# Performance work log

Hardware: AMD Instinct MI355X
Metric: run time of the kernel (lower is better)

Reference implementation:

```python
import jax, jax.numpy as jnp
import numpy as np

B, S, D, H = 2, 2048, 1024, 16
HD = D // H
LN_EPS = 1e-5


def setup_inputs() -> dict:
    key = jax.random.key(0)
    ks = jax.random.split(key, 8)
    inv = 1.0 / np.sqrt(D)
    return {
        "embedded": jax.random.normal(ks[0], (B, S, D), dtype=jnp.float32),
        "Wq": jax.random.normal(ks[1], (D, D), dtype=jnp.float32) * inv,
        "bq": jax.random.normal(ks[2], (D,), dtype=jnp.float32) * 0.01,
        "Wk": jax.random.normal(ks[3], (D, D), dtype=jnp.float32) * inv,
        "bk": jax.random.normal(ks[4], (D,), dtype=jnp.float32) * 0.01,
        "Wv": jax.random.normal(ks[5], (D, D), dtype=jnp.float32) * inv,
        "bv": jax.random.normal(ks[6], (D,), dtype=jnp.float32) * 0.01,
        "gamma": jnp.ones((D,), dtype=jnp.float32),
        "beta": jnp.zeros((D,), dtype=jnp.float32),
    }


def reference(embedded, Wq, bq, Wk, bk, Wv, bv, gamma, beta):
    b, s, d = embedded.shape
    # QKV projections (torch Linear: x @ W^T + b)
    q = embedded @ Wq.T + bq
    k = embedded @ Wk.T + bk
    v = embedded @ Wv.T + bv
    # [b, s, H, hd] -> [b, H, s, hd]
    q = q.reshape(b, s, H, HD).transpose(0, 2, 1, 3)
    k = k.reshape(b, s, H, HD).transpose(0, 2, 1, 3)
    v = v.reshape(b, s, H, HD).transpose(0, 2, 1, 3)
    # scores [b, H, s, s]
    qk = jnp.einsum("bhqd,bhkd->bhqk", q, k)
    # NaN scrub -> -inf (original: qk[qk != qk] = -inf)
    qk = jnp.where(jnp.isnan(qk), -jnp.inf, qk)
    # NOTE: original scales by sqrt(shape[-1]) == sqrt(seq_len), not head_dim
    qk = qk / jnp.float32(np.sqrt(s))
    p = jax.nn.softmax(qk, axis=-1)
    p = jnp.where(jnp.isnan(p), 0.0, p)
    v = jnp.where(jnp.isnan(v), 0.0, v)
    # post-softmax upper-triangular (incl. diagonal) mask, no renormalization
    mask = jnp.triu(jnp.ones((s, s), dtype=p.dtype), k=0)
    p = p * mask
    z = jnp.einsum("bhqk,bhkd->bhqd", p, v)  # [b, H, s, hd]
    # original does a raw .view(b, s, -1) on contiguous [b,h,s,hd] (no transpose)
    z = z.reshape(b, s, d)
    # residual + LayerNorm
    x = embedded + z
    mu = jnp.mean(x, axis=-1, keepdims=True)
    var = jnp.mean(jnp.square(x - mu), axis=-1, keepdims=True)
    out = (x - mu) * jax.lax.rsqrt(var + LN_EPS) * gamma + beta
    return out
```

## Files before the change

kernel.cpp:

```cpp
#include <hip/hip_runtime.h>
#include <hip/hip_bf16.h>
#include <math.h>

typedef unsigned short ushort_t;
typedef unsigned char uchar_t;
typedef __attribute__((ext_vector_type(8))) short short8;
typedef __attribute__((ext_vector_type(4))) float f32x4;

struct __align__(8) us4 { ushort_t u[4]; };

__device__ __forceinline__ ushort_t f2bf(float x) {
  union { float f; unsigned u; } c; c.f = x;
  unsigned r = c.u + 0x7FFFu + ((c.u >> 16) & 1u);
  return (ushort_t)(r >> 16);
}
__device__ __forceinline__ float bf2f(ushort_t b) {
  union { unsigned u; float f; } c; c.u = ((unsigned)b) << 16;
  return c.f;
}

__global__ __launch_bounds__(256) void cvt_kernel(const float* __restrict__ src,
                                                  ushort_t* __restrict__ dst, int n) {
  int i = (blockIdx.x * 256 + threadIdx.x) * 4;
  if (i < n) {
    f32x4 v = *(const f32x4*)(src + i);
    us4 o;
    o.u[0] = f2bf(v[0]); o.u[1] = f2bf(v[1]); o.u[2] = f2bf(v[2]); o.u[3] = f2bf(v[3]);
    *(us4*)(dst + i) = o;
  }
}

struct QkvArgs {
  const ushort_t* X;
  const ushort_t* W0; const ushort_t* W1; const ushort_t* W2;
  const float* b0; const float* b1; const float* b2;
  ushort_t* o0; ushort_t* o1; ushort_t* o2;
};

__global__ __launch_bounds__(256) void qkv_gemm(QkvArgs a) {
  __shared__ __align__(16) ushort_t As[128 * 32];
  __shared__ __align__(16) ushort_t Bs[128 * 32];
  const int z = blockIdx.z;
  const ushort_t* W  = (z == 0) ? a.W0 : ((z == 1) ? a.W1 : a.W2);
  const float* bias  = (z == 0) ? a.b0 : ((z == 1) ? a.b1 : a.b2);
  ushort_t* out      = (z == 0) ? a.o0 : ((z == 1) ? a.o1 : a.o2);
  const int swz = (z == 1) ? 7 : 0;
  const int mBase = blockIdx.x * 128;
  const int nBase = blockIdx.y * 128;
  const int tid  = threadIdx.x;
  const int lane = tid & 63;
  const int w    = tid >> 6;
  const int wm   = w >> 1, wn = w & 1;
  const int quad = lane >> 4;
  const int l15  = lane & 15;

  f32x4 acc[4][4] = {};

  const int srow = lane >> 2;
  const int scol = (lane & 3) * 8;
  const ushort_t* gA0 = a.X + (mBase + srow) * 1024 + scol;
  const ushort_t* gB0 = W   + (nBase + srow) * 1024 + scol;

  for (int k0 = 0; k0 < 1024; k0 += 32) {
#pragma unroll
    for (int p = 0; p < 2; ++p) {
      int rr = (w * 2 + p) * 16;
      __builtin_amdgcn_global_load_lds(
          (const __attribute__((address_space(1))) void*)(gA0 + rr * 1024 + k0),
          (__attribute__((address_space(3))) void*)(As + (w * 2 + p) * 512), 16, 0, 0);
      __builtin_amdgcn_global_load_lds(
          (const __attribute__((address_space(1))) void*)(gB0 + rr * 1024 + k0),
          (__attribute__((address_space(3))) void*)(Bs + (w * 2 + p) * 512), 16, 0, 0);
    }
    __syncthreads();
    short8 af[4], bfr[4];
#pragma unroll
    for (int mi = 0; mi < 4; ++mi)
      af[mi] = *(const short8*)(As + (wm * 64 + mi * 16 + l15) * 32 + quad * 8);
#pragma unroll
    for (int ni = 0; ni < 4; ++ni)
      bfr[ni] = *(const short8*)(Bs + (wn * 64 + ni * 16 + l15) * 32 + quad * 8);
#pragma unroll
    for (int mi = 0; mi < 4; ++mi)
#pragma unroll
      for (int ni = 0; ni < 4; ++ni)
        acc[mi][ni] = __builtin_amdgcn_mfma_f32_16x16x32_bf16(af[mi], bfr[ni], acc[mi][ni], 0, 0, 0);
    __syncthreads();
  }

#pragma unroll
  for (int ni = 0; ni < 4; ++ni) {
    int n = nBase + wn * 64 + ni * 16 + l15;
    float bv = bias[n];
    int h = n >> 6, hd = n & 63;
    int hdHi = hd >> 3, hdLo = hd & 7;
#pragma unroll
    for (int mi = 0; mi < 4; ++mi) {
      int m0 = mBase + wm * 64 + mi * 16 + quad * 4;
#pragma unroll
      for (int r = 0; r < 4; ++r) {
        int m = m0 + r;
        int bb = m >> 11, s = m & 2047;
        int hdw = (((hdHi ^ (s & swz)) << 3) | hdLo);
        out[((bb * 16 + h) * 2048 + s) * 64 + hdw] = f2bf(acc[mi][ni][r] + bv);
      }
    }
  }
}

__global__ __launch_bounds__(256) void tr_kernel(const ushort_t* __restrict__ vb,
                                                 uchar_t* __restrict__ vT) {
  __shared__ uchar_t Ls[64 * 68];
  int bh = blockIdx.y;
  int s0 = blockIdx.x * 64;
  int tid = threadIdx.x;
  const ushort_t* vp = vb + (size_t)bh * 131072;
  uchar_t* op = vT + (size_t)bh * 131072;
#pragma unroll
  for (int p = 0; p < 2; ++p) {
    int c = p * 256 + tid;
    int row = c >> 3, u = c & 7;
    short8 x = *(const short8*)(vp + (size_t)(s0 + row) * 64 + u * 8);
    float f0 = bf2f((ushort_t)x[0]), f1 = bf2f((ushort_t)x[1]);
    float f2 = bf2f((ushort_t)x[2]), f3 = bf2f((ushort_t)x[3]);
    float f4 = bf2f((ushort_t)x[4]), f5 = bf2f((ushort_t)x[5]);
    float f6 = bf2f((ushort_t)x[6]), f7 = bf2f((ushort_t)x[7]);
    unsigned int lo = __builtin_amdgcn_cvt_pk_fp8_f32(f0, f1, 0, false);
    lo = __builtin_amdgcn_cvt_pk_fp8_f32(f2, f3, lo, true);
    unsigned int hi = __builtin_amdgcn_cvt_pk_fp8_f32(f4, f5, 0, false);
    hi = __builtin_amdgcn_cvt_pk_fp8_f32(f6, f7, hi, true);
    *(unsigned int*)(Ls + row * 68 + u * 8)     = lo;
    *(unsigned int*)(Ls + row * 68 + u * 8 + 4) = hi;
  }
  __syncthreads();
#pragma unroll
  for (int p = 0; p < 4; ++p) {
    int oc = p * 256 + tid;
    int hd = oc >> 4, sc = oc & 15;
    unsigned int v = 0;
#pragma unroll
    for (int i = 0; i < 4; ++i)
      v |= ((unsigned int)Ls[(sc * 4 + i) * 68 + hd]) << (8 * i);
    int u = ((s0 & 64) >> 4) + (sc >> 2);
    int dest = (s0 & ~127) + ((u ^ (hd & 7)) * 16) + (sc & 3) * 4;
    *(unsigned int*)(op + (size_t)hd * 2048 + dest) = v;
  }
}

__global__ __launch_bounds__(256) void attn_kernel(const ushort_t* __restrict__ qb,
                                                   const ushort_t* __restrict__ kb,
                                                   const uchar_t* __restrict__ vT,
                                                   ushort_t* __restrict__ zb) {
  __shared__ __align__(16) ushort_t Ks[128 * 64];
  __shared__ __align__(16) uchar_t  Vt[64 * 128];
  __shared__ __align__(16) uchar_t  Ps[128 * 128];
  const int bh   = blockIdx.y;
  const int qblk = blockIdx.x * 128;
  const int tid  = threadIdx.x;
  const int lane = tid & 63;
  const int w    = tid >> 6;
  const int quad = lane >> 4;
  const int l15  = lane & 15;
  const int l7   = l15 & 7;
  const float cexp = 0.02209708691f * 1.44269504089f;

  const ushort_t* qpage = qb + (size_t)bh * (2048 * 64);
  const ushort_t* kpage = kb + (size_t)bh * (2048 * 64);
  const uchar_t*  vpage = vT + (size_t)bh * (64 * 2048);

  short8 qf[2][2];
#pragma unroll
  for (int nb = 0; nb < 2; ++nb) {
    int qg = qblk + w * 32 + nb * 16 + l15;
#pragma unroll
    for (int kd = 0; kd < 2; ++kd)
      qf[nb][kd] = *(const short8*)(qpage + (size_t)qg * 64 + kd * 32 + quad * 8);
  }

  float psum[2] = {0.f, 0.f};
  f32x4 o[4][2] = {};

  for (int kt = 0; kt < 2048; kt += 128) {
    const bool needV = (kt + 127 >= qblk);
    const bool needP = (kt + 127 >= qblk + w * 32);
    __syncthreads();

#pragma unroll
    for (int p = 0; p < 4; ++p) {
      int j = w * 4 + p;
      __builtin_amdgcn_global_load_lds(
          (const __attribute__((address_space(1))) void*)(kpage + (size_t)kt * 64 + j * 512 + lane * 8),
          (__attribute__((address_space(3))) void*)(Ks + j * 512), 16, 0, 0);
    }
    if (needV) {
#pragma unroll
      for (int p = 0; p < 2; ++p) {
        int j = w * 2 + p;
        __builtin_amdgcn_global_load_lds(
            (const __attribute__((address_space(1))) void*)(vpage + (size_t)(j * 8 + (lane >> 3)) * 2048 + kt + (lane & 7) * 16),
            (__attribute__((address_space(3))) void*)(Vt + j * 1024), 16, 0, 0);
      }
    }
    __syncthreads();

#pragma unroll
    for (int mb = 0; mb < 8; ++mb) {
      const ushort_t* krow = Ks + (mb * 16 + l15) * 64;
      short8 kf0 = *(const short8*)(krow + ((0 + quad) ^ l7) * 8);
      short8 kf1 = *(const short8*)(krow + ((4 + quad) ^ l7) * 8);
      f32x4 s0 = {}, s1 = {};
      s0 = __builtin_amdgcn_mfma_f32_16x16x32_bf16(kf0, qf[0][0], s0, 0, 0, 0);
      s0 = __builtin_amdgcn_mfma_f32_16x16x32_bf16(kf1, qf[0][1], s0, 0, 0, 0);
      s1 = __builtin_amdgcn_mfma_f32_16x16x32_bf16(kf0, qf[1][0], s1, 0, 0, 0);
      s1 = __builtin_amdgcn_mfma_f32_16x16x32_bf16(kf1, qf[1][1], s1, 0, 0, 0);
      const int keyb = kt + mb * 16 + quad * 4;
#pragma unroll
      for (int nb = 0; nb < 2; ++nb) {
        f32x4 s = nb ? s1 : s0;
        float p0 = __builtin_amdgcn_exp2f(s[0] * cexp);
        float p1 = __builtin_amdgcn_exp2f(s[1] * cexp);
        float p2 = __builtin_amdgcn_exp2f(s[2] * cexp);
        float p3 = __builtin_amdgcn_exp2f(s[3] * cexp);
        psum[nb] += (p0 + p1) + (p2 + p3);
        if (needP) {
          int qg = qblk + w * 32 + nb * 16 + l15;
          float m0 = (keyb + 0 >= qg) ? p0 : 0.f;
          float m1 = (keyb + 1 >= qg) ? p1 : 0.f;
          float m2 = (keyb + 2 >= qg) ? p2 : 0.f;
          float m3 = (keyb + 3 >= qg) ? p3 : 0.f;
          unsigned int pk = __builtin_amdgcn_cvt_pk_fp8_f32(m0, m1, 0, false);
          pk = __builtin_amdgcn_cvt_pk_fp8_f32(m2, m3, pk, true);
          *(unsigned int*)(Ps + (w * 32 + nb * 16 + l15) * 128 + ((mb ^ l7) * 16) + quad * 4) = pk;
        }
      }
    }

    if (needP) {
#pragma unroll
      for (int kd = 0; kd < 4; ++kd) {
        const int un = ((kd * 2 + (quad >> 1)) ^ l7) * 16 + (quad & 1) * 8;
        long long pf0 = *(const long long*)(Ps + (w * 32 + l15) * 128 + un);
        long long pf1 = *(const long long*)(Ps + (w * 32 + 16 + l15) * 128 + un);
#pragma unroll
        for (int mb = 0; mb < 4; ++mb) {
          long long vf = *(const long long*)(Vt + (mb * 16 + l15) * 128 + un);
          o[mb][0] = __builtin_amdgcn_mfma_f32_16x16x32_fp8_fp8(vf, pf0, o[mb][0], 0, 0, 0);
          o[mb][1] = __builtin_amdgcn_mfma_f32_16x16x32_fp8_fp8(vf, pf1, o[mb][1], 0, 0, 0);
        }
      }
    }
  }

#pragma unroll
  for (int nb = 0; nb < 2; ++nb) {
    psum[nb] += __shfl_xor(psum[nb], 16, 64);
    psum[nb] += __shfl_xor(psum[nb], 32, 64);
    float rl = 1.0f / psum[nb];
    int qg = qblk + w * 32 + nb * 16 + l15;
#pragma unroll
    for (int mb = 0; mb < 4; ++mb)
#pragma unroll
      for (int r = 0; r < 4; ++r) {
        int hd = mb * 16 + quad * 4 + r;
        zb[((size_t)bh * 2048 + qg) * 64 + hd] = f2bf(o[mb][nb][r] * rl);
      }
  }
}

__global__ __launch_bounds__(256) void ln_kernel(const float* __restrict__ emb,
                                                 const ushort_t* __restrict__ zb,
                                                 const float* __restrict__ gamma,
                                                 const float* __restrict__ beta,
                                                 float* __restrict__ out) {
  __shared__ float red[2][4];
  int row = blockIdx.x;
  int b = row >> 11, s = row & 2047;
  int h = s >> 7;
  int siHi = (s & 127) << 4;
  int tid = threadIdx.x;
  int dcol = tid * 4;
  int si = siHi | (dcol >> 6);
  int j = dcol & 63;

  f32x4 e4 = *(const f32x4*)(emb + (size_t)row * 1024 + dcol);
  us4 z4 = *(const us4*)(zb + (((size_t)(b * 16 + h) * 2048 + si) * 64 + j));
  float x0 = e4[0] + bf2f(z4.u[0]);
  float x1 = e4[1] + bf2f(z4.u[1]);
  float x2 = e4[2] + bf2f(z4.u[2]);
  float x3 = e4[3] + bf2f(z4.u[3]);

  float sum = x0 + x1 + x2 + x3;
  float sq  = x0 * x0 + x1 * x1 + x2 * x2 + x3 * x3;
#pragma unroll
  for (int off = 1; off <= 32; off <<= 1) {
    sum += __shfl_xor(sum, off, 64);
    sq  += __shfl_xor(sq,  off, 64);
  }
  int wv = tid >> 6;
  if ((tid & 63) == 0) { red[0][wv] = sum; red[1][wv] = sq; }
  __syncthreads();
  float ts = red[0][0] + red[0][1] + red[0][2] + red[0][3];
  float tq = red[1][0] + red[1][1] + red[1][2] + red[1][3];
  float mu = ts * (1.0f / 1024.0f);
  float var = tq * (1.0f / 1024.0f) - mu * mu;
  float rsig = rsqrtf(var + 1e-5f);

  f32x4 g4 = *(const f32x4*)(gamma + dcol);
  f32x4 b4 = *(const f32x4*)(beta + dcol);
  f32x4 o4;
  o4[0] = (x0 - mu) * rsig * g4[0] + b4[0];
  o4[1] = (x1 - mu) * rsig * g4[1] + b4[1];
  o4[2] = (x2 - mu) * rsig * g4[2] + b4[2];
  o4[3] = (x3 - mu) * rsig * g4[3] + b4[3];
  *(f32x4*)(out + (size_t)row * 1024 + dcol) = o4;
}

extern "C" void kernel_launch(void* const* d_in, const int* in_sizes, int n_in,
                              void* d_out, int out_size, void* d_ws, size_t ws_size,
                              hipStream_t stream) {
  (void)in_sizes; (void)n_in; (void)out_size; (void)ws_size;
  const float* emb   = (const float*)d_in[0];
  const float* Wq    = (const float*)d_in[1];
  const float* bq    = (const float*)d_in[2];
  const float* Wk    = (const float*)d_in[3];
  const float* bk    = (const float*)d_in[4];
  const float* Wv    = (const float*)d_in[5];
  const float* bv    = (const float*)d_in[6];
  const float* gamma = (const float*)d_in[7];
  const float* beta  = (const float*)d_in[8];
  float* out = (float*)d_out;

  char* ws = (char*)d_ws;
  ushort_t* Xbf  = (ushort_t*)(ws);
  ushort_t* Wqb  = (ushort_t*)(ws + 8388608);
  ushort_t* Wkb  = (ushort_t*)(ws + 10485760);
  ushort_t* Wvb  = (ushort_t*)(ws + 12582912);
  ushort_t* qbuf = (ushort_t*)(ws + 14680064);
  ushort_t* kbuf = (ushort_t*)(ws + 23068672);
  ushort_t* vbuf = (ushort_t*)(ws + 31457280);
  ushort_t* zbuf = (ushort_t*)(ws + 31457280);
  uchar_t*  vTb  = (uchar_t*)(ws + 39845888);

  cvt_kernel<<<4096, 256, 0, stream>>>(emb, Xbf, 4194304);
  cvt_kernel<<<1024, 256, 0, stream>>>(Wq, Wqb, 1048576);
  cvt_kernel<<<1024, 256, 0, stream>>>(Wk, Wkb, 1048576);
  cvt_kernel<<<1024, 256, 0, stream>>>(Wv, Wvb, 1048576);

  QkvArgs a;
  a.X = Xbf;
  a.W0 = Wqb; a.W1 = Wkb; a.W2 = Wvb;
  a.b0 = bq;  a.b1 = bk;  a.b2 = bv;
  a.o0 = qbuf; a.o1 = kbuf; a.o2 = vbuf;
  qkv_gemm<<<dim3(32, 8, 3), 256, 0, stream>>>(a);

  tr_kernel<<<dim3(32, 32), 256, 0, stream>>>(vbuf, vTb);

  attn_kernel<<<dim3(16, 32), 256, 0, stream>>>(qbuf, kbuf, vTb, zbuf);

  ln_kernel<<<4096, 256, 0, stream>>>(emb, zbuf, gamma, beta, out);
}
```

Measured before the change: 197.8 us.

## Split attention key range across two blocks and combine partial outputs

Attention is split along the key dimension into two halves via a third grid dimension, each writing a normalized bf16 partial output and its row sum. A new combine kernel merges the halves weighted by their sums. This doubles the number of attention blocks to improve GPU occupancy and load balance. The cost is an extra launch, extra partial-output memory traffic, and an extra bf16 rounding. It is only enabled when the workspace is large enough.

```diff
diff --git a/kernel.cpp b/kernel.cpp
--- a/kernel.cpp
+++ b/kernel.cpp
@@ -150,11 +150,16 @@
 __global__ __launch_bounds__(256) void attn_kernel(const ushort_t* __restrict__ qb,
                                                    const ushort_t* __restrict__ kb,
                                                    const uchar_t* __restrict__ vT,
-                                                   ushort_t* __restrict__ zb) {
+                                                   ushort_t* __restrict__ outO,
+                                                   float* __restrict__ outPs,
+                                                   int split) {
   __shared__ __align__(16) ushort_t Ks[128 * 64];
   __shared__ __align__(16) uchar_t  Vt[64 * 128];
   __shared__ __align__(16) uchar_t  Ps[128 * 128];
   const int bh   = blockIdx.y;
+  const int half = blockIdx.z;
+  const int kz   = half * 1024;
+  const int kend = split ? (kz + 1024) : 2048;
   const int qblk = blockIdx.x * 128;
   const int tid  = threadIdx.x;
   const int lane = tid & 63;
@@ -180,7 +185,7 @@
   float psum[2] = {0.f, 0.f};
   f32x4 o[4][2] = {};
 
-  for (int kt = 0; kt < 2048; kt += 128) {
+  for (int kt = kz; kt < kend; kt += 128) {
     const bool needV = (kt + 127 >= qblk);
     const bool needP = (kt + 127 >= qblk + w * 32);
     __syncthreads();
@@ -257,14 +262,38 @@
     psum[nb] += __shfl_xor(psum[nb], 32, 64);
     float rl = 1.0f / psum[nb];
     int qg = qblk + w * 32 + nb * 16 + l15;
+    size_t base = (((size_t)(half * 32 + bh) * 2048) + qg) * 64;
 #pragma unroll
     for (int mb = 0; mb < 4; ++mb)
 #pragma unroll
       for (int r = 0; r < 4; ++r) {
         int hd = mb * 16 + quad * 4 + r;
-        zb[((size_t)bh * 2048 + qg) * 64 + hd] = f2bf(o[mb][nb][r] * rl);
-      }
-  }
+        outO[base + hd] = f2bf(o[mb][nb][r] * rl);
+      }
+    if (split && quad == 0)
+      outPs[(half * 32 + bh) * 2048 + qg] = psum[nb];
+  }
+}
+
+__global__ __launch_bounds__(256) void comb_kernel(const ushort_t* __restrict__ Op,
+                                                   const float* __restrict__ Psm,
+                                                   ushort_t* __restrict__ zb) {
+  int t = blockIdx.x * 256 + threadIdx.x;
+  int chunk = t & 15;
+  int q  = (t >> 4) & 2047;
+  int bh = t >> 15;
+  float ps0 = Psm[bh * 2048 + q];
+  float ps1 = Psm[(32 + bh) * 2048 + q];
+  float rt = 1.0f / (ps0 + ps1);
+  size_t i0 = (((size_t)bh * 2048) + q) * 64 + chunk * 4;
+  size_t i1 = (((size_t)(32 + bh) * 2048) + q) * 64 + chunk * 4;
+  us4 a = *(const us4*)(Op + i0);
+  us4 b = *(const us4*)(Op + i1);
+  us4 r;
+#pragma unroll
+  for (int j = 0; j < 4; ++j)
+    r.u[j] = f2bf((ps0 * bf2f(a.u[j]) + ps1 * bf2f(b.u[j])) * rt);
+  *(us4*)(zb + i0) = r;
 }
 
 __global__ __launch_bounds__(256) void ln_kernel(const float* __restrict__ emb,
@@ -318,7 +347,7 @@
 extern "C" void kernel_launch(void* const* d_in, const int* in_sizes, int n_in,
                               void* d_out, int out_size, void* d_ws, size_t ws_size,
                               hipStream_t stream) {
-  (void)in_sizes; (void)n_in; (void)out_size; (void)ws_size;
+  (void)in_sizes; (void)n_in; (void)out_size;
   const float* emb   = (const float*)d_in[0];
   const float* Wq    = (const float*)d_in[1];
   const float* bq    = (const float*)d_in[2];
@@ -340,6 +369,9 @@
   ushort_t* vbuf = (ushort_t*)(ws + 31457280);
   ushort_t* zbuf = (ushort_t*)(ws + 31457280);
   uchar_t*  vTb  = (uchar_t*)(ws + 39845888);
+  ushort_t* Opart = (ushort_t*)(ws + 44040192);
+  float*    Psum  = (float*)(ws + 77594624);
+  const bool split = ws_size >= 78118912u;
 
   cvt_kernel<<<4096, 256, 0, stream>>>(emb, Xbf, 4194304);
   cvt_kernel<<<1024, 256, 0, stream>>>(Wq, Wqb, 1048576);
@@ -355,7 +387,12 @@
 
   tr_kernel<<<dim3(32, 32), 256, 0, stream>>>(vbuf, vTb);
 
-  attn_kernel<<<dim3(16, 32), 256, 0, stream>>>(qbuf, kbuf, vTb, zbuf);
+  if (split) {
+    attn_kernel<<<dim3(16, 32, 2), 256, 0, stream>>>(qbuf, kbuf, vTb, Opart, Psum, 1);
+    comb_kernel<<<4096, 256, 0, stream>>>(Opart, Psum, zbuf);
+  } else {
+    attn_kernel<<<dim3(16, 32, 1), 256, 0, stream>>>(qbuf, kbuf, vTb, zbuf, (float*)ws, 0);
+  }
 
   ln_kernel<<<4096, 256, 0, stream>>>(emb, zbuf, gamma, beta, out);
 }
```

After: 202.5 us. 1.02x slower.

## Double-buffer K and V tiles in LDS to prefetch the next key block

Applied to the files above, without the earlier changes.

The attention kernel now keeps two LDS buffers each for the K and V tiles. It issues the async global-to-LDS loads for the next 128-key block right after the barrier, then computes on the current block. This is meant to hide global load latency behind the QK^T, softmax and PV MFMA work, and it drops one barrier per iteration. In exchange LDS use per block rises from about 40KB to 64KB, which could limit occupancy, and the compiler may insert conservative vmcnt waits before LDS reads that cancel the overlap.

```diff
diff --git a/kernel.cpp b/kernel.cpp
--- a/kernel.cpp
+++ b/kernel.cpp
@@ -151,8 +151,8 @@
                                                    const ushort_t* __restrict__ kb,
                                                    const uchar_t* __restrict__ vT,
                                                    ushort_t* __restrict__ zb) {
-  __shared__ __align__(16) ushort_t Ks[128 * 64];
-  __shared__ __align__(16) uchar_t  Vt[64 * 128];
+  __shared__ __align__(16) ushort_t Ks[2][128 * 64];
+  __shared__ __align__(16) uchar_t  Vt[2][64 * 128];
   __shared__ __align__(16) uchar_t  Ps[128 * 128];
   const int bh   = blockIdx.y;
   const int qblk = blockIdx.x * 128;
@@ -180,72 +180,97 @@
   float psum[2] = {0.f, 0.f};
   f32x4 o[4][2] = {};
 
-  for (int kt = 0; kt < 2048; kt += 128) {
-    const bool needV = (kt + 127 >= qblk);
-    const bool needP = (kt + 127 >= qblk + w * 32);
-    __syncthreads();
-
-#pragma unroll
-    for (int p = 0; p < 4; ++p) {
-      int j = w * 4 + p;
+#pragma unroll
+  for (int p = 0; p < 4; ++p) {
+    int j = w * 4 + p;
+    __builtin_amdgcn_global_load_lds(
+        (const __attribute__((address_space(1))) void*)(kpage + (size_t)j * 512 + lane * 8),
+        (__attribute__((address_space(3))) void*)(Ks[0] + j * 512), 16, 0, 0);
+  }
+  if (127 >= qblk) {
+#pragma unroll
+    for (int p = 0; p < 2; ++p) {
+      int j = w * 2 + p;
       __builtin_amdgcn_global_load_lds(
-          (const __attribute__((address_space(1))) void*)(kpage + (size_t)kt * 64 + j * 512 + lane * 8),
-          (__attribute__((address_space(3))) void*)(Ks + j * 512), 16, 0, 0);
+          (const __attribute__((address_space(1))) void*)(vpage + (size_t)(j * 8 + (lane >> 3)) * 2048 + (lane & 7) * 16),
+          (__attribute__((address_space(3))) void*)(Vt[0] + j * 1024), 16, 0, 0);
     }
-    if (needV) {
-#pragma unroll
-      for (int p = 0; p < 2; ++p) {
-        int j = w * 2 + p;
-        __builtin_amdgcn_global_load_lds(
-            (const __attribute__((address_space(1))) void*)(vpage + (size_t)(j * 8 + (lane >> 3)) * 2048 + kt + (lane & 7) * 16),
-            (__attribute__((address_space(3))) void*)(Vt + j * 1024), 16, 0, 0);
-      }
-    }
-    __syncthreads();
-
-#pragma unroll
-    for (int mb = 0; mb < 8; ++mb) {
-      const ushort_t* krow = Ks + (mb * 16 + l15) * 64;
-      short8 kf0 = *(const short8*)(krow + ((0 + quad) ^ l7) * 8);
-      short8 kf1 = *(const short8*)(krow + ((4 + quad) ^ l7) * 8);
-      f32x4 s0 = {}, s1 = {};
-      s0 = __builtin_amdgcn_mfma_f32_16x16x32_bf16(kf0, qf[0][0], s0, 0, 0, 0);
-      s0 = __builtin_amdgcn_mfma_f32_16x16x32_bf16(kf1, qf[0][1], s0, 0, 0, 0);
-      s1 = __builtin_amdgcn_mfma_f32_16x16x32_bf16(kf0, qf[1][0], s1, 0, 0, 0);
-      s1 = __builtin_amdgcn_mfma_f32_16x16x32_bf16(kf1, qf[1][1], s1, 0, 0, 0);
-      const int keyb = kt + mb * 16 + quad * 4;
-#pragma unroll
-      for (int nb = 0; nb < 2; ++nb) {
-        f32x4 s = nb ? s1 : s0;
-        float p0 = __builtin_amdgcn_exp2f(s[0] * cexp);
-        float p1 = __builtin_amdgcn_exp2f(s[1] * cexp);
-        float p2 = __builtin_amdgcn_exp2f(s[2] * cexp);
-        float p3 = __builtin_amdgcn_exp2f(s[3] * cexp);
-        psum[nb] += (p0 + p1) + (p2 + p3);
-        if (needP) {
-          int qg = qblk + w * 32 + nb * 16 + l15;
-          float m0 = (keyb + 0 >= qg) ? p0 : 0.f;
-          float m1 = (keyb + 1 >= qg) ? p1 : 0.f;
-          float m2 = (keyb + 2 >= qg) ? p2 : 0.f;
-          float m3 = (keyb + 3 >= qg) ? p3 : 0.f;
-          unsigned int pk = __builtin_amdgcn_cvt_pk_fp8_f32(m0, m1, 0, false);
-          pk = __builtin_amdgcn_cvt_pk_fp8_f32(m2, m3, pk, true);
-          *(unsigned int*)(Ps + (w * 32 + nb * 16 + l15) * 128 + ((mb ^ l7) * 16) + quad * 4) = pk;
+  }
+
+  for (int kt2 = 0; kt2 < 2048; kt2 += 256) {
+#pragma unroll
+    for (int ph = 0; ph < 2; ++ph) {
+      const int kt = kt2 + ph * 128;
+      const ushort_t* KsB = Ks[ph];
+      const uchar_t*  VtB = Vt[ph];
+      const bool needP = (kt + 127 >= qblk + w * 32);
+
+      __syncthreads();
+
+      const int ktn = kt + 128;
+      if (ktn < 2048) {
+#pragma unroll
+        for (int p = 0; p < 4; ++p) {
+          int j = w * 4 + p;
+          __builtin_amdgcn_global_load_lds(
+              (const __attribute__((address_space(1))) void*)(kpage + (size_t)ktn * 64 + j * 512 + lane * 8),
+              (__attribute__((address_space(3))) void*)(Ks[ph ^ 1] + j * 512), 16, 0, 0);
         }
-      }
-    }
-
-    if (needP) {
-#pragma unroll
-      for (int kd = 0; kd < 4; ++kd) {
-        const int un = ((kd * 2 + (quad >> 1)) ^ l7) * 16 + (quad & 1) * 8;
-        long long pf0 = *(const long long*)(Ps + (w * 32 + l15) * 128 + un);
-        long long pf1 = *(const long long*)(Ps + (w * 32 + 16 + l15) * 128 + un);
-#pragma unroll
-        for (int mb = 0; mb < 4; ++mb) {
-          long long vf = *(const long long*)(Vt + (mb * 16 + l15) * 128 + un);
-          o[mb][0] = __builtin_amdgcn_mfma_f32_16x16x32_fp8_fp8(vf, pf0, o[mb][0], 0, 0, 0);
-          o[mb][1] = __builtin_amdgcn_mfma_f32_16x16x32_fp8_fp8(vf, pf1, o[mb][1], 0, 0, 0);
+        if (ktn + 127 >= qblk) {
+#pragma unroll
+          for (int p = 0; p < 2; ++p) {
+            int j = w * 2 + p;
+            __builtin_amdgcn_global_load_lds(
+                (const __attribute__((address_space(1))) void*)(vpage + (size_t)(j * 8 + (lane >> 3)) * 2048 + ktn + (lane & 7) * 16),
+                (__attribute__((address_space(3))) void*)(Vt[ph ^ 1] + j * 1024), 16, 0, 0);
+          }
+        }
+      }
+
+#pragma unroll
+      for (int mb = 0; mb < 8; ++mb) {
+        const ushort_t* krow = KsB + (mb * 16 + l15) * 64;
+        short8 kf0 = *(const short8*)(krow + ((0 + quad) ^ l7) * 8);
+        short8 kf1 = *(const short8*)(krow + ((4 + quad) ^ l7) * 8);
+        f32x4 s0 = {}, s1 = {};
+        s0 = __builtin_amdgcn_mfma_f32_16x16x32_bf16(kf0, qf[0][0], s0, 0, 0, 0);
+        s0 = __builtin_amdgcn_mfma_f32_16x16x32_bf16(kf1, qf[0][1], s0, 0, 0, 0);
+        s1 = __builtin_amdgcn_mfma_f32_16x16x32_bf16(kf0, qf[1][0], s1, 0, 0, 0);
+        s1 = __builtin_amdgcn_mfma_f32_16x16x32_bf16(kf1, qf[1][1], s1, 0, 0, 0);
+        const int keyb = kt + mb * 16 + quad * 4;
+#pragma unroll
+        for (int nb = 0; nb < 2; ++nb) {
+          f32x4 s = nb ? s1 : s0;
+          float p0 = __builtin_amdgcn_exp2f(s[0] * cexp);
+          float p1 = __builtin_amdgcn_exp2f(s[1] * cexp);
+          float p2 = __builtin_amdgcn_exp2f(s[2] * cexp);
+          float p3 = __builtin_amdgcn_exp2f(s[3] * cexp);
+          psum[nb] += (p0 + p1) + (p2 + p3);
+          if (needP) {
+            int qg = qblk + w * 32 + nb * 16 + l15;
+            float m0 = (keyb + 0 >= qg) ? p0 : 0.f;
+            float m1 = (keyb + 1 >= qg) ? p1 : 0.f;
+            float m2 = (keyb + 2 >= qg) ? p2 : 0.f;
+            float m3 = (keyb + 3 >= qg) ? p3 : 0.f;
+            unsigned int pk = __builtin_amdgcn_cvt_pk_fp8_f32(m0, m1, 0, false);
+            pk = __builtin_amdgcn_cvt_pk_fp8_f32(m2, m3, pk, true);
+            *(unsigned int*)(Ps + (w * 32 + nb * 16 + l15) * 128 + ((mb ^ l7) * 16) + quad * 4) = pk;
+          }
+        }
+      }
+
+      if (needP) {
+#pragma unroll
+        for (int kd = 0; kd < 4; ++kd) {
+          const int un = ((kd * 2 + (quad >> 1)) ^ l7) * 16 + (quad & 1) * 8;
+          long long pf0 = *(const long long*)(Ps + (w * 32 + l15) * 128 + un);
+          long long pf1 = *(const long long*)(Ps + (w * 32 + 16 + l15) * 128 + un);
+#pragma unroll
+          for (int mb = 0; mb < 4; ++mb) {
+            long long vf = *(const long long*)(VtB + (mb * 16 + l15) * 128 + un);
+            o[mb][0] = __builtin_amdgcn_mfma_f32_16x16x32_fp8_fp8(vf, pf0, o[mb][0], 0, 0, 0);
+            o[mb][1] = __builtin_amdgcn_mfma_f32_16x16x32_fp8_fp8(vf, pf1, o[mb][1], 0, 0, 0);
+          }
         }
       }
     }
```

New measurement: 227.6 us. +15.1%, slower.

## Fuse V fp8 transpose into QKV GEMM epilogue and merge conversion launches

Applied to the files above, without the earlier changes.

The V projection epilogue now converts accumulators directly to fp8 and writes them in the transposed, swizzled layout the attention kernel expects. This removes the separate transpose kernel and the bf16 V round trip through memory. The four fp32-to-bf16 conversion launches are merged into one kernel that picks its source by block index, which cuts launch overhead. In exchange, V is quantized straight from fp32 instead of via bf16, which could change rounding slightly, and the epilogue writes 4-byte scattered stores.

```diff
diff --git a/kernel.cpp b/kernel.cpp
--- a/kernel.cpp
+++ b/kernel.cpp
@@ -19,22 +19,30 @@
   return c.f;
 }
 
-__global__ __launch_bounds__(256) void cvt_kernel(const float* __restrict__ src,
-                                                  ushort_t* __restrict__ dst, int n) {
-  int i = (blockIdx.x * 256 + threadIdx.x) * 4;
-  if (i < n) {
-    f32x4 v = *(const f32x4*)(src + i);
-    us4 o;
-    o.u[0] = f2bf(v[0]); o.u[1] = f2bf(v[1]); o.u[2] = f2bf(v[2]); o.u[3] = f2bf(v[3]);
-    *(us4*)(dst + i) = o;
-  }
+struct CvtArgs {
+  const float* s0; const float* s1; const float* s2; const float* s3;
+  ushort_t* d0; ushort_t* d1; ushort_t* d2; ushort_t* d3;
+};
+
+__global__ __launch_bounds__(256) void cvt4_kernel(CvtArgs a) {
+  int blk = blockIdx.x;
+  const float* src; ushort_t* dst; int off;
+  if (blk < 4096)      { src = a.s0; dst = a.d0; off = blk; }
+  else if (blk < 5120) { src = a.s1; dst = a.d1; off = blk - 4096; }
+  else if (blk < 6144) { src = a.s2; dst = a.d2; off = blk - 5120; }
+  else                 { src = a.s3; dst = a.d3; off = blk - 6144; }
+  int idx = (off * 256 + threadIdx.x) * 4;
+  f32x4 v = *(const f32x4*)(src + idx);
+  us4 o;
+  o.u[0] = f2bf(v[0]); o.u[1] = f2bf(v[1]); o.u[2] = f2bf(v[2]); o.u[3] = f2bf(v[3]);
+  *(us4*)(dst + idx) = o;
 }
 
 struct QkvArgs {
   const ushort_t* X;
   const ushort_t* W0; const ushort_t* W1; const ushort_t* W2;
   const float* b0; const float* b1; const float* b2;
-  ushort_t* o0; ushort_t* o1; ushort_t* o2;
+  ushort_t* oQ; ushort_t* oK; uchar_t* oV;
 };
 
 __global__ __launch_bounds__(256) void qkv_gemm(QkvArgs a) {
@@ -43,8 +51,6 @@
   const int z = blockIdx.z;
   const ushort_t* W  = (z == 0) ? a.W0 : ((z == 1) ? a.W1 : a.W2);
   const float* bias  = (z == 0) ? a.b0 : ((z == 1) ? a.b1 : a.b2);
-  ushort_t* out      = (z == 0) ? a.o0 : ((z == 1) ? a.o1 : a.o2);
-  const int swz = (z == 1) ? 7 : 0;
   const int mBase = blockIdx.x * 128;
   const int nBase = blockIdx.y * 128;
   const int tid  = threadIdx.x;
@@ -88,62 +94,44 @@
     __syncthreads();
   }
 
-#pragma unroll
-  for (int ni = 0; ni < 4; ++ni) {
-    int n = nBase + wn * 64 + ni * 16 + l15;
-    float bv = bias[n];
-    int h = n >> 6, hd = n & 63;
-    int hdHi = hd >> 3, hdLo = hd & 7;
-#pragma unroll
-    for (int mi = 0; mi < 4; ++mi) {
-      int m0 = mBase + wm * 64 + mi * 16 + quad * 4;
-#pragma unroll
-      for (int r = 0; r < 4; ++r) {
-        int m = m0 + r;
-        int bb = m >> 11, s = m & 2047;
-        int hdw = (((hdHi ^ (s & swz)) << 3) | hdLo);
-        out[((bb * 16 + h) * 2048 + s) * 64 + hdw] = f2bf(acc[mi][ni][r] + bv);
-      }
-    }
-  }
-}
-
-__global__ __launch_bounds__(256) void tr_kernel(const ushort_t* __restrict__ vb,
-                                                 uchar_t* __restrict__ vT) {
-  __shared__ uchar_t Ls[64 * 68];
-  int bh = blockIdx.y;
-  int s0 = blockIdx.x * 64;
-  int tid = threadIdx.x;
-  const ushort_t* vp = vb + (size_t)bh * 131072;
-  uchar_t* op = vT + (size_t)bh * 131072;
-#pragma unroll
-  for (int p = 0; p < 2; ++p) {
-    int c = p * 256 + tid;
-    int row = c >> 3, u = c & 7;
-    short8 x = *(const short8*)(vp + (size_t)(s0 + row) * 64 + u * 8);
-    float f0 = bf2f((ushort_t)x[0]), f1 = bf2f((ushort_t)x[1]);
-    float f2 = bf2f((ushort_t)x[2]), f3 = bf2f((ushort_t)x[3]);
-    float f4 = bf2f((ushort_t)x[4]), f5 = bf2f((ushort_t)x[5]);
-    float f6 = bf2f((ushort_t)x[6]), f7 = bf2f((ushort_t)x[7]);
-    unsigned int lo = __builtin_amdgcn_cvt_pk_fp8_f32(f0, f1, 0, false);
-    lo = __builtin_amdgcn_cvt_pk_fp8_f32(f2, f3, lo, true);
-    unsigned int hi = __builtin_amdgcn_cvt_pk_fp8_f32(f4, f5, 0, false);
-    hi = __builtin_amdgcn_cvt_pk_fp8_f32(f6, f7, hi, true);
-    *(unsigned int*)(Ls + row * 68 + u * 8)     = lo;
-    *(unsigned int*)(Ls + row * 68 + u * 8 + 4) = hi;
-  }
-  __syncthreads();
-#pragma unroll
-  for (int p = 0; p < 4; ++p) {
-    int oc = p * 256 + tid;
-    int hd = oc >> 4, sc = oc & 15;
-    unsigned int v = 0;
-#pragma unroll
-    for (int i = 0; i < 4; ++i)
-      v |= ((unsigned int)Ls[(sc * 4 + i) * 68 + hd]) << (8 * i);
-    int u = ((s0 & 64) >> 4) + (sc >> 2);
-    int dest = (s0 & ~127) + ((u ^ (hd & 7)) * 16) + (sc & 3) * 4;
-    *(unsigned int*)(op + (size_t)hd * 2048 + dest) = v;
+  if (z < 2) {
+    ushort_t* out = (z == 0) ? a.oQ : a.oK;
+    const int swz = (z == 1) ? 7 : 0;
+#pragma unroll
+    for (int ni = 0; ni < 4; ++ni) {
+      int n = nBase + wn * 64 + ni * 16 + l15;
+      float bv = bias[n];
+      int h = n >> 6, hd = n & 63;
+      int hdHi = hd >> 3, hdLo = hd & 7;
+#pragma unroll
+      for (int mi = 0; mi < 4; ++mi) {
+        int m0 = mBase + wm * 64 + mi * 16 + quad * 4;
+#pragma unroll
+        for (int r = 0; r < 4; ++r) {
+          int m = m0 + r;
+          int bb = m >> 11, s = m & 2047;
+          int hdw = (((hdHi ^ (s & swz)) << 3) | hdLo);
+          out[((bb * 16 + h) * 2048 + s) * 64 + hdw] = f2bf(acc[mi][ni][r] + bv);
+        }
+      }
+    }
+  } else {
+#pragma unroll
+    for (int ni = 0; ni < 4; ++ni) {
+      int n = nBase + wn * 64 + ni * 16 + l15;
+      float bv = bias[n];
+      int h = n >> 6, hd = n & 63;
+#pragma unroll
+      for (int mi = 0; mi < 4; ++mi) {
+        int m0 = mBase + wm * 64 + mi * 16 + quad * 4;
+        int bb = m0 >> 11, s0 = m0 & 2047;
+        unsigned int pk = __builtin_amdgcn_cvt_pk_fp8_f32(acc[mi][ni][0] + bv, acc[mi][ni][1] + bv, 0, false);
+        pk = __builtin_amdgcn_cvt_pk_fp8_f32(acc[mi][ni][2] + bv, acc[mi][ni][3] + bv, pk, true);
+        size_t addr = (size_t)(bb * 16 + h) * 131072 + hd * 2048 +
+                      (s0 & ~127) + ((((s0 >> 4) & 7) ^ (hd & 7)) << 4) + (s0 & 15);
+        *(unsigned int*)(a.oV + addr) = pk;
+      }
+    }
   }
 }
 
@@ -337,24 +325,21 @@
   ushort_t* Wvb  = (ushort_t*)(ws + 12582912);
   ushort_t* qbuf = (ushort_t*)(ws + 14680064);
   ushort_t* kbuf = (ushort_t*)(ws + 23068672);
-  ushort_t* vbuf = (ushort_t*)(ws + 31457280);
-  ushort_t* zbuf = (ushort_t*)(ws + 31457280);
-  uchar_t*  vTb  = (uchar_t*)(ws + 39845888);
-
-  cvt_kernel<<<4096, 256, 0, stream>>>(emb, Xbf, 4194304);
-  cvt_kernel<<<1024, 256, 0, stream>>>(Wq, Wqb, 1048576);
-  cvt_kernel<<<1024, 256, 0, stream>>>(Wk, Wkb, 1048576);
-  cvt_kernel<<<1024, 256, 0, stream>>>(Wv, Wvb, 1048576);
+  uchar_t*  vTb  = (uchar_t*)(ws + 31457280);
+  ushort_t* zbuf = (ushort_t*)(ws + 35651584);
+
+  CvtArgs c;
+  c.s0 = emb; c.s1 = Wq; c.s2 = Wk; c.s3 = Wv;
+  c.d0 = Xbf; c.d1 = Wqb; c.d2 = Wkb; c.d3 = Wvb;
+  cvt4_kernel<<<7168, 256, 0, stream>>>(c);
 
   QkvArgs a;
   a.X = Xbf;
   a.W0 = Wqb; a.W1 = Wkb; a.W2 = Wvb;
   a.b0 = bq;  a.b1 = bk;  a.b2 = bv;
-  a.o0 = qbuf; a.o1 = kbuf; a.o2 = vbuf;
+  a.oQ = qbuf; a.oK = kbuf; a.oV = vTb;
   qkv_gemm<<<dim3(32, 8, 3), 256, 0, stream>>>(a);
 
-  tr_kernel<<<dim3(32, 32), 256, 0, stream>>>(vbuf, vTb);
-
   attn_kernel<<<dim3(16, 32), 256, 0, stream>>>(qbuf, kbuf, vTb, zbuf);
 
   ln_kernel<<<4096, 256, 0, stream>>>(emb, zbuf, gamma, beta, out);
```

Result: no change. 201.4 us (+1.8%).
